# Kernel tuning notes

Hardware: AMD Instinct MI355X
Metric: run time of the kernel (lower is better)

## Reference

```python
import jax, jax.numpy as jnp
import numpy as np
from jax import lax

MU = 0.9      # params['momentum']
S = 0.1       # params['stepsize']
BETA = 0.999  # params['rnn_beta']
EPS = 1e-16   # self.eps

B, SEQ, IN, H = 64, 512, 512, 1024
G = 4 * H  # gates_size


def setup_inputs() -> dict:
    key = jax.random.key(0)
    ks = jax.random.split(key, 5)
    return {
        "x": jax.random.normal(ks[0], (B, SEQ, IN), dtype=jnp.float32),
        "weight_ih": jax.random.normal(ks[1], (IN, G), dtype=jnp.float32) * 0.05,
        "weight_hh": jax.random.normal(ks[2], (H, G), dtype=jnp.float32) * 0.05,
        "bias_ih": jax.random.normal(ks[3], (G,), dtype=jnp.float32) * 0.05,
        "bias_hh": jax.random.normal(ks[4], (G,), dtype=jnp.float32) * 0.05,
        "h0": jnp.zeros((B, H), dtype=jnp.float32),
        "c0": jnp.zeros((B, H), dtype=jnp.float32),
        "v0": jnp.zeros((B, G), dtype=jnp.float32),
        "m0": jnp.zeros((B, G), dtype=jnp.float32),
    }


def reference(x, weight_ih, weight_hh, bias_ih, bias_hh, h0, c0, v0, m0):
    # Precompute the input-to-gates projection for all timesteps in one GEMM.
    # grad_t = x_t @ W_ih + b_ih  -> [S, B, 4H] for scan
    grad_all = jnp.swapaxes(jnp.einsum('bsi,ig->bsg', x, weight_ih) + bias_ih, 0, 1)

    def step(carry, grad):
        h, c, v, m = carry
        v = MU * v + S * grad                       # momentum buffer
        m = BETA * m + (1.0 - BETA) * (grad * grad)  # second-moment buffer
        gates = v / (jnp.sqrt(m) + EPS) + h @ weight_hh + bias_hh
        i_g, f_g, g_g, o_g = jnp.split(gates, 4, axis=1)
        i_g = jax.nn.sigmoid(i_g)
        f_g = jax.nn.sigmoid(f_g)
        g_g = jnp.tanh(g_g)
        o_g = jax.nn.sigmoid(o_g)
        c = c * f_g + i_g * g_g
        h = o_g * jnp.tanh(c)
        return (h, c, v, m), h

    (h, c, v, m), ys = lax.scan(step, (h0, c0, v0, m0), grad_all)
    layer_output = jnp.swapaxes(ys, 0, 1)  # [B, S, H]
    return layer_output, h, c, v, m
```

## Files before the change

kernel.cpp:

```cpp
#include <hip/hip_runtime.h>
#include <cstdint>
#include <cstddef>

#define BB   64
#define SEQL 512
#define INF  512
#define HID  1024
#define GG   4096

#define MU_    0.9f
#define SSTEP_ 0.1f
#define BETA_  0.999f
#define EPS_   1e-16f
#define SCL    2048.0f
#define ISCL   (1.0f / 2048.0f)

#define NWGC  64
#define NWGP  128
#define NWG_TOT (NWGC + NWGP)
#define NTHR  1024
#define WLDS  131072
#define RLDS  32768
#define SMEM_BYTES (WLDS + RLDS)

typedef unsigned short u16;
typedef unsigned int   u32;
typedef unsigned long long u64;
typedef _Float16 half8 __attribute__((ext_vector_type(8)));
typedef float f32x4 __attribute__((ext_vector_type(4)));
typedef u32 u32x4 __attribute__((ext_vector_type(4)));

__device__ __forceinline__ f32x4 mfma16(half8 a, half8 b, f32x4 c) {
  return __builtin_amdgcn_mfma_f32_16x16x32_f16(a, b, c, 0, 0, 0);
}
__device__ __forceinline__ void fsplit(float v, _Float16& hi, _Float16& lo) {
  hi = (_Float16)v;
  lo = (_Float16)((v - (float)hi) * SCL);
}
__device__ __forceinline__ u32 coh_load32(const u32* p) {
  return __hip_atomic_load(p, __ATOMIC_RELAXED, __HIP_MEMORY_SCOPE_AGENT);
}
__device__ __forceinline__ void coh_store32(u32* p, u32 v) {
  __hip_atomic_store(p, v, __ATOMIC_RELAXED, __HIP_MEMORY_SCOPE_AGENT);
}
__device__ __forceinline__ void coh_store64(u64* p, u64 v) {
  __hip_atomic_store(p, v, __ATOMIC_RELAXED, __HIP_MEMORY_SCOPE_AGENT);
}
__device__ __forceinline__ void coh_storef(float* p, float v) {
  __hip_atomic_store(p, v, __ATOMIC_RELAXED, __HIP_MEMORY_SCOPE_AGENT);
}

#define GLD8(o0,o1,o2,o3,o4,o5,o6,o7,addr)                      \
  asm volatile(                                                 \
    "global_load_dwordx4 %0, %8, off sc0 sc1\n\t"               \
    "global_load_dwordx4 %1, %8, off offset:64 sc0 sc1\n\t"     \
    "global_load_dwordx4 %2, %8, off offset:128 sc0 sc1\n\t"    \
    "global_load_dwordx4 %3, %8, off offset:192 sc0 sc1\n\t"    \
    "global_load_dwordx4 %4, %8, off offset:256 sc0 sc1\n\t"    \
    "global_load_dwordx4 %5, %8, off offset:320 sc0 sc1\n\t"    \
    "global_load_dwordx4 %6, %8, off offset:384 sc0 sc1\n\t"    \
    "global_load_dwordx4 %7, %8, off offset:448 sc0 sc1"        \
    : "=&v"(o0), "=&v"(o1), "=&v"(o2), "=&v"(o3),               \
      "=&v"(o4), "=&v"(o5), "=&v"(o6), "=&v"(o7)                \
    : "v"(addr))

#define GLDU4(d0,d1,d2,d3,a0,a1,a2,a3)                          \
  asm volatile(                                                 \
    "global_load_dword %0, %4, off sc0 sc1\n\t"                 \
    "global_load_dword %1, %5, off sc0 sc1\n\t"                 \
    "global_load_dword %2, %6, off sc0 sc1\n\t"                 \
    "global_load_dword %3, %7, off sc0 sc1"                     \
    : "=&v"(d0), "=&v"(d1), "=&v"(d2), "=&v"(d3)                \
    : "v"(a0), "v"(a1), "v"(a2), "v"(a3))

#define HIMF(Hk, kk)                                                        \
  {                                                                         \
    half8 ah = __builtin_bit_cast(half8, Hk);                               \
    const _Float16* wb = Wf + (size_t)((kq * 8 + (kk)) * 4) * 512 + lane * 8;\
    a0 = mfma16(ah, *(const half8*)(wb), a0);                               \
    a1 = mfma16(ah, *(const half8*)(wb + 512), a1);                         \
    a2 = mfma16(ah, *(const half8*)(wb + 1024), a2);                        \
    a3 = mfma16(ah, *(const half8*)(wb + 1536), a3);                        \
  }

__global__ __launch_bounds__(256) void transpose_split(const float* __restrict__ src,
                                                       _Float16* __restrict__ dhi,
                                                       _Float16* __restrict__ dlo,
                                                       int R, int C) {
  __shared__ float tile[32][33];
  int c0 = blockIdx.x * 32, r0 = blockIdx.y * 32;
  int tx = threadIdx.x & 31, ty = threadIdx.x >> 5;
#pragma unroll
  for (int i = 0; i < 32; i += 8)
    tile[ty + i][tx] = src[(size_t)(r0 + ty + i) * C + (c0 + tx)];
  __syncthreads();
#pragma unroll
  for (int i = 0; i < 32; i += 8) {
    float v = tile[tx][ty + i];
    _Float16 hi, lo;
    fsplit(v, hi, lo);
    size_t o = (size_t)(c0 + ty + i) * R + (r0 + tx);
    dhi[o] = hi;
    dlo[o] = lo;
  }
}

__global__ __launch_bounds__(256) void split_x(const float* __restrict__ x,
                                               _Float16* __restrict__ xs) {
  size_t i = (size_t)blockIdx.x * 256 + threadIdx.x;
  size_t e = i * 8;
  size_t r = e / INF, col = e % INF;
  f32x4 v0 = *(const f32x4*)(x + e);
  f32x4 v1 = *(const f32x4*)(x + e + 4);
  half8 hi, lo;
#pragma unroll
  for (int j = 0; j < 4; j++) {
    _Float16 h_, l_;
    fsplit(v0[j], h_, l_); hi[j] = h_; lo[j] = l_;
    fsplit(v1[j], h_, l_); hi[4 + j] = h_; lo[4 + j] = l_;
  }
  _Float16* dst = xs + r * 2 * INF + col;
  *(half8*)(dst) = hi;
  *(half8*)(dst + INF) = lo;
}

__global__ __launch_bounds__(256) void init_state(const float* __restrict__ h0,
                                                  const float* __restrict__ c0,
                                                  const float* __restrict__ v0,
                                                  const float* __restrict__ m0,
                                                  float* __restrict__ co,
                                                  float* __restrict__ vo,
                                                  float* __restrict__ mo,
                                                  _Float16* __restrict__ hhi) {
  int i = blockIdx.x * 256 + threadIdx.x;
  if (i < BB * GG) { vo[i] = v0[i]; mo[i] = m0[i]; }
  if (i < BB * HID) {
    co[i] = c0[i];
    hhi[i] = (_Float16)h0[i];
  }
}

__global__ __attribute__((amdgpu_flat_work_group_size(NTHR, NTHR),
                          amdgpu_waves_per_eu(4, 4))) void rnn_fused(
    const _Float16* __restrict__ xs,
    const _Float16* __restrict__ whi,
    const _Float16* __restrict__ wlo,
    const float* __restrict__ bih,
    float* __restrict__ u,
    const _Float16* __restrict__ whh_hi,
    const float* __restrict__ bhh,
    _Float16* __restrict__ hA, _Float16* __restrict__ hB,
    float* __restrict__ lout, float* __restrict__ hout,
    float* __restrict__ cout,
    float* __restrict__ vst, float* __restrict__ mst,
    u32* __restrict__ flags, int t0, int T) {
  extern __shared__ char smem[];
  int tid = threadIdx.x;
  int wave = tid >> 6, lane = tid & 63;
  int l15 = lane & 15, lg = lane >> 4;

  if (blockIdx.x < NWGC) {
    _Float16* Wf = (_Float16*)smem;
    float* red = (float*)(smem + WLDS);
    u16* hpk = (u16*)(smem + WLDS);
    int bt = wave >> 2, kq = wave & 3;
    int nb = blockIdx.x;

    for (int s = tid; s < 8192; s += NTHR) {
      int ln = s & 63, rest = s >> 6;
      int rt = rest & 3, kk = (rest >> 2) & 7, kq2 = rest >> 5;
      int grow = rt * HID + nb * 16 + (ln & 15);
      int k = kq2 * 256 + kk * 32 + (ln >> 4) * 8;
      *(half8*)(Wf + (size_t)s * 8) = *(const half8*)(whh_hi + (size_t)grow * HID + k);
    }

    int bo = tid >> 4, j = tid & 15;
    int en = nb * 16 + j;
    int within = bo & 15, btE = bo >> 4;
    int wsl = (((within >> 2) + j) & 3) * 4 + (within & 3);
    float bh_[4], creg;
#pragma unroll
    for (int q = 0; q < 4; q++) bh_[q] = bhh[q * HID + en];
    creg = cout[(size_t)bo * HID + en];
    u64 hOffB = (u64)(((bt * 16 + l15) * HID + kq * 256 + lg * 8) * 2);
    u64 hAB = (u64)(uintptr_t)hA + hOffB;
    u64 hBB = (u64)(uintptr_t)hB + hOffB;
    int sb = tid >> 2, ss = tid & 3;
    u64* stA = (u64*)(hA + (size_t)sb * HID + nb * 16) + ss;
    u64* stB = (u64*)(hB + (size_t)sb * HID + nb * 16) + ss;
    u64 ubT = (u64)(uintptr_t)u + (((size_t)bo * GG) + en) * 4;
    __syncthreads();

    if (wave == 0) {
      u32 tp = (u32)(t0 + (T < 2 ? T : 2));
      const u32* p0 = flags + (size_t)(NWGC + 2 * lane) * 32;
      while (!__all(coh_load32(p0) >= tp && coh_load32(p0 + 32) >= tp))
        __builtin_amdgcn_s_sleep(1);
    }
    __syncthreads();
    float uv0, uv1, uv2, uv3;
    GLDU4(uv0, uv1, uv2, uv3, ubT, ubT + 4096, ubT + 8192, ubT + 12288);
    asm volatile("s_waitcnt vmcnt(0)"
                 : "+v"(uv0), "+v"(uv1), "+v"(uv2), "+v"(uv3) :: "memory");
    float uv[4] = {uv0, uv1, uv2, uv3};

    for (int tt = 0; tt < T; ++tt) {
      int gt = t0 + tt;
      u64 rB = (gt & 1) ? hBB : hAB;

      u32x4 H0, H1, H2, H3, H4, H5, H6, H7;
      GLD8(H0, H1, H2, H3, H4, H5, H6, H7, rB);
      asm volatile("s_waitcnt vmcnt(0)" ::: "memory");
      __builtin_amdgcn_sched_barrier(0);

      f32x4 a0 = {}, a1 = {}, a2 = {}, a3 = {};
      HIMF(H0, 0) HIMF(H1, 1) HIMF(H2, 2) HIMF(H3, 3)
      HIMF(H4, 4) HIMF(H5, 5) HIMF(H6, 6) HIMF(H7, 7)

      int kqh = kq >> 1;
      int p = (lg + l15) & 3;
      int sB0 = (((bt * 2 + kqh) * 4 + 0) * 16 + l15) * 16 + p * 4;
      int sB1 = (((bt * 2 + kqh) * 4 + 1) * 16 + l15) * 16 + p * 4;
      int sB2 = (((bt * 2 + kqh) * 4 + 2) * 16 + l15) * 16 + p * 4;
      int sB3 = (((bt * 2 + kqh) * 4 + 3) * 16 + l15) * 16 + p * 4;
      if (kq & 1) {
        *(f32x4*)(red + sB0) = a0;
        *(f32x4*)(red + sB1) = a1;
        *(f32x4*)(red + sB2) = a2;
        *(f32x4*)(red + sB3) = a3;
      }
      __syncthreads();
      if (!(kq & 1)) {
        *(f32x4*)(red + sB0) = a0 + *(const f32x4*)(red + sB0);
        *(f32x4*)(red + sB1) = a1 + *(const f32x4*)(red + sB1);
        *(f32x4*)(red + sB2) = a2 + *(const f32x4*)(red + sB2);
        *(f32x4*)(red + sB3) = a3 + *(const f32x4*)(red + sB3);
      }
      float uvN0 = 0, uvN1 = 0, uvN2 = 0, uvN3 = 0;
      if (tt + 1 < T) {
        u64 ubn = ubT + ((u64)(tt + 1) * ((u64)BB * GG * 4));
        GLDU4(uvN0, uvN1, uvN2, uvN3, ubn, ubn + 4096, ubn + 8192, ubn + 12288);
      }
      __syncthreads();

      float gate[4];
#pragma unroll
      for (int q = 0; q < 4; q++) {
        float rec = red[(((btE * 2 + 0) * 4 + q) * 16 + j) * 16 + wsl] +
                    red[(((btE * 2 + 1) * 4 + q) * 16 + j) * 16 + wsl];
        gate[q] = uv[q] + rec + bh_[q];
      }
      float ig = 1.0f / (1.0f + expf(-gate[0]));
      float fg = 1.0f / (1.0f + expf(-gate[1]));
      float gg = tanhf(gate[2]);
      float og = 1.0f / (1.0f + expf(-gate[3]));
      creg = creg * fg + ig * gg;
      float hh = og * tanhf(creg);
      __syncthreads();

      lout[((size_t)bo * SEQL + gt) * HID + en] = hh;
      hpk[bo * 16 + j] = __builtin_bit_cast(u16, (_Float16)hh);
      if (gt == SEQL - 1) hout[(size_t)bo * HID + en] = hh;
      if (tt == T - 1)    cout[(size_t)bo * HID + en] = creg;
      __syncthreads();

      if (tid < 256) {
        u64 val = *(const u64*)(hpk + sb * 16 + ss * 4);
        coh_store64((gt & 1) ? stA : stB, val);
      }

      if (tt + 1 < T) {
        asm volatile("s_waitcnt vmcnt(0)"
                     : "+v"(uvN0), "+v"(uvN1), "+v"(uvN2), "+v"(uvN3) :: "memory");
        __syncthreads();
        u32 target = (u32)(t0 + tt + 1);
        if (tid == 0) coh_store32(flags + (size_t)nb * 32, target);
        if (wave == 0) {
          const u32* f0 = flags + (size_t)lane * 32;
          while (!__all(coh_load32(f0) >= target))
            __builtin_amdgcn_s_sleep(1);
        } else if (wave == 1) {
          u32 t2 = (u32)(t0 + (tt + 3 < T ? tt + 3 : T));
          const u32* p0 = flags + (size_t)(NWGC + 2 * lane) * 32;
          while (!__all(coh_load32(p0) >= t2 && coh_load32(p0 + 32) >= t2))
            __builtin_amdgcn_s_sleep(1);
        }
        __syncthreads();
        uv[0] = uvN0; uv[1] = uvN1; uv[2] = uvN2; uv[3] = uvN3;
      }
    }
  } else {
    float* pred = (float*)smem;
    int pid = blockIdx.x - NWGC;
    int btp = pid & 3;
    int n0 = (pid >> 2) * 128;
    int nt = wave & 7, kh = wave >> 3;

    const _Float16* xa = xs + (size_t)(btp * 16 + l15) * SEQL * (2 * INF)
                            + kh * 256 + lg * 8;
    const _Float16* whp = whi + (size_t)(n0 + nt * 16 + l15) * INF + kh * 256 + lg * 8;
    const _Float16* wlp = wlo + (size_t)(n0 + nt * 16 + l15) * INF + kh * 256 + lg * 8;
    float* pp = pred + (((kh * 8 + nt) * 16 + l15) * 16 + lg * 4);

    int b_l = tid >> 6, g_l = tid & 63;
    int bg = btp * 16 + b_l;
    int g0 = n0 + g_l, g1 = n0 + g_l + 64;
    size_t gi0 = (size_t)bg * GG + g0, gi1 = (size_t)bg * GG + g1;
    float vr0 = vst[gi0], vr1 = vst[gi1];
    float mr0 = mst[gi0], mr1 = mst[gi1];
    float bi0 = bih[g0], bi1 = bih[g1];
    int nt0 = g_l >> 4, c0i = g_l & 15;
    int nt1 = (g_l + 64) >> 4, c1i = g_l & 15;
    __syncthreads();

    for (int tt = 0; tt < T; ++tt) {
      const _Float16* xt = xa + (size_t)(t0 + tt) * (2 * INF);
      f32x4 aM = {}, aL = {};
#pragma unroll
      for (int kk = 0; kk < 256; kk += 32) {
        half8 ah = *(const half8*)(xt + kk);
        half8 al = *(const half8*)(xt + INF + kk);
        half8 bh = *(const half8*)(whp + kk);
        half8 bl = *(const half8*)(wlp + kk);
        aM = mfma16(ah, bh, aM);
        aL = mfma16(al, bh, aL);
        aL = mfma16(ah, bl, aL);
      }
      f32x4 cb;
#pragma unroll
      for (int i2 = 0; i2 < 4; ++i2) cb[i2] = aM[i2] + aL[i2] * ISCL;
      *(f32x4*)pp = cb;
      __syncthreads();

      float rec0 = pred[((0 + nt0) * 16 + c0i) * 16 + b_l] +
                   pred[((8 + nt0) * 16 + c0i) * 16 + b_l];
      float rec1 = pred[((0 + nt1) * 16 + c1i) * 16 + b_l] +
                   pred[((8 + nt1) * 16 + c1i) * 16 + b_l];
      float gr0 = rec0 + bi0, gr1 = rec1 + bi1;
      vr0 = MU_ * vr0 + SSTEP_ * gr0;
      mr0 = BETA_ * mr0 + (1.0f - BETA_) * gr0 * gr0;
      vr1 = MU_ * vr1 + SSTEP_ * gr1;
      mr1 = BETA_ * mr1 + (1.0f - BETA_) * gr1 * gr1;
      float* ub = u + ((size_t)tt * BB + bg) * GG;
      coh_storef(ub + g0, vr0 / (sqrtf(mr0) + EPS_));
      coh_storef(ub + g1, vr1 / (sqrtf(mr1) + EPS_));
      if (tt == T - 1) {
        vst[gi0] = vr0; vst[gi1] = vr1;
        mst[gi0] = mr0; mst[gi1] = mr1;
      }
      asm volatile("s_waitcnt vmcnt(0)" ::: "memory");
      __syncthreads();
      if (tid == 0)
        coh_store32(flags + (size_t)(NWGC + pid) * 32, (u32)(t0 + tt + 1));
    }
  }
}

extern "C" void kernel_launch(void* const* d_in, const int* in_sizes, int n_in,
                              void* d_out, int out_size, void* d_ws, size_t ws_size,
                              hipStream_t stream) {
  const float* x   = (const float*)d_in[0];
  const float* wih = (const float*)d_in[1];
  const float* whh = (const float*)d_in[2];
  const float* bih = (const float*)d_in[3];
  const float* bhh = (const float*)d_in[4];
  const float* h0  = (const float*)d_in[5];
  const float* c0  = (const float*)d_in[6];
  const float* v0  = (const float*)d_in[7];
  const float* m0  = (const float*)d_in[8];

  float* out  = (float*)d_out;
  float* lout = out;
  float* hout = out + (size_t)BB * SEQL * HID;
  float* cout = hout + (size_t)BB * HID;
  float* vout = cout + (size_t)BB * HID;
  float* mout = vout + (size_t)BB * GG;

  char* ws = (char*)d_ws;
  size_t o = 0;
  _Float16* wih_hi = (_Float16*)(ws + o); o += (size_t)GG * INF * 2;
  _Float16* wih_lo = (_Float16*)(ws + o); o += (size_t)GG * INF * 2;
  _Float16* whh_hi = (_Float16*)(ws + o); o += (size_t)GG * HID * 2;
  _Float16* whh_lo = (_Float16*)(ws + o); o += (size_t)GG * HID * 2;
  _Float16* xs     = (_Float16*)(ws + o); o += (size_t)BB * SEQL * 2 * INF * 2;
  _Float16* hA     = (_Float16*)(ws + o); o += (size_t)BB * HID * 2;
  _Float16* hB     = (_Float16*)(ws + o); o += (size_t)BB * HID * 2;
  o = (o + 255) & ~(size_t)255;
  u32* flags = (u32*)(ws + o); o += (size_t)NWG_TOT * 32 * 4;
  float* U = (float*)(ws + o);

  const size_t STEP_BYTES = (size_t)BB * GG * sizeof(float);
  size_t cap = (ws_size > o) ? (ws_size - o) / STEP_BYTES : 1;
  if (cap < 1) cap = 1;
  int Tc = (int)(cap < (size_t)SEQL ? cap : (size_t)SEQL);

  split_x<<<(BB * SEQL * INF / 8) / 256, 256, 0, stream>>>(x, xs);
  transpose_split<<<dim3(GG / 32, INF / 32), 256, 0, stream>>>(wih, wih_hi, wih_lo, INF, GG);
  transpose_split<<<dim3(GG / 32, HID / 32), 256, 0, stream>>>(whh, whh_hi, whh_lo, HID, GG);
  init_state<<<(BB * GG) / 256, 256, 0, stream>>>(h0, c0, v0, m0, cout, vout, mout, hA);
  hipMemsetAsync(flags, 0, (size_t)NWG_TOT * 32 * 4, stream);

  for (int t0 = 0; t0 < SEQL; t0 += Tc) {
    int T = (SEQL - t0 < Tc) ? (SEQL - t0) : Tc;
    rnn_fused<<<NWG_TOT, NTHR, SMEM_BYTES, stream>>>(
        xs, wih_hi, wih_lo, bih, U, whh_hi, bhh,
        hA, hB, lout, hout, cout, vout, mout, flags, t0, T);
  }
}
```

Baseline: 4.585 ms.

## Replace per-step flag barrier with timestep-tagged hidden-state words polled directly

Each fp16 hidden value is stored in a 32-bit word with the timestep tag in the upper half. Consumer workgroups spin on the hidden-state loads until every tag matches the current step, which removes the separate flag store, all-workgroup flag poll and extra syncthreads per timestep. The next-step U prefetch is issued earlier and the producer-progress wait is moved after the MFMAs. This doubles the bytes read and written for h each step and adds unpack work. Correctness depends on the per-word tagging holding across buffer reuse.

Measured after the change: 6.119 ms. 33.5% more time.

```diff
diff --git a/kernel.cpp b/kernel.cpp
--- a/kernel.cpp
+++ b/kernel.cpp
@@ -50,19 +50,29 @@
   __hip_atomic_store(p, v, __ATOMIC_RELAXED, __HIP_MEMORY_SCOPE_AGENT);
 }
 
-#define GLD8(o0,o1,o2,o3,o4,o5,o6,o7,addr)                      \
-  asm volatile(                                                 \
-    "global_load_dwordx4 %0, %8, off sc0 sc1\n\t"               \
-    "global_load_dwordx4 %1, %8, off offset:64 sc0 sc1\n\t"     \
-    "global_load_dwordx4 %2, %8, off offset:128 sc0 sc1\n\t"    \
-    "global_load_dwordx4 %3, %8, off offset:192 sc0 sc1\n\t"    \
-    "global_load_dwordx4 %4, %8, off offset:256 sc0 sc1\n\t"    \
-    "global_load_dwordx4 %5, %8, off offset:320 sc0 sc1\n\t"    \
-    "global_load_dwordx4 %6, %8, off offset:384 sc0 sc1\n\t"    \
-    "global_load_dwordx4 %7, %8, off offset:448 sc0 sc1"        \
-    : "=&v"(o0), "=&v"(o1), "=&v"(o2), "=&v"(o3),               \
-      "=&v"(o4), "=&v"(o5), "=&v"(o6), "=&v"(o7)                \
-    : "v"(addr))
+#define GLD16(P0,P1,P2,P3,P4,P5,P6,P7,P8,P9,Pa,Pb,Pc,Pd,Pe,Pf,PA)  \
+  asm volatile(                                                     \
+    "global_load_dwordx4 %0, %16, off sc0 sc1\n\t"                  \
+    "global_load_dwordx4 %1, %16, off offset:16 sc0 sc1\n\t"        \
+    "global_load_dwordx4 %2, %16, off offset:128 sc0 sc1\n\t"       \
+    "global_load_dwordx4 %3, %16, off offset:144 sc0 sc1\n\t"       \
+    "global_load_dwordx4 %4, %16, off offset:256 sc0 sc1\n\t"       \
+    "global_load_dwordx4 %5, %16, off offset:272 sc0 sc1\n\t"       \
+    "global_load_dwordx4 %6, %16, off offset:384 sc0 sc1\n\t"       \
+    "global_load_dwordx4 %7, %16, off offset:400 sc0 sc1\n\t"       \
+    "global_load_dwordx4 %8, %16, off offset:512 sc0 sc1\n\t"       \
+    "global_load_dwordx4 %9, %16, off offset:528 sc0 sc1\n\t"       \
+    "global_load_dwordx4 %10, %16, off offset:640 sc0 sc1\n\t"      \
+    "global_load_dwordx4 %11, %16, off offset:656 sc0 sc1\n\t"      \
+    "global_load_dwordx4 %12, %16, off offset:768 sc0 sc1\n\t"      \
+    "global_load_dwordx4 %13, %16, off offset:784 sc0 sc1\n\t"      \
+    "global_load_dwordx4 %14, %16, off offset:896 sc0 sc1\n\t"      \
+    "global_load_dwordx4 %15, %16, off offset:912 sc0 sc1"          \
+    : "=&v"(P0), "=&v"(P1), "=&v"(P2), "=&v"(P3),                   \
+      "=&v"(P4), "=&v"(P5), "=&v"(P6), "=&v"(P7),                   \
+      "=&v"(P8), "=&v"(P9), "=&v"(Pa), "=&v"(Pb),                   \
+      "=&v"(Pc), "=&v"(Pd), "=&v"(Pe), "=&v"(Pf)                    \
+    : "v"(PA))
 
 #define GLDU4(d0,d1,d2,d3,a0,a1,a2,a3)                          \
   asm volatile(                                                 \
@@ -73,14 +83,18 @@
     : "=&v"(d0), "=&v"(d1), "=&v"(d2), "=&v"(d3)                \
     : "v"(a0), "v"(a1), "v"(a2), "v"(a3))
 
-#define HIMF(Hk, kk)                                                        \
+#define UNPK_MFMA(W0, W1, kk)                                               \
   {                                                                         \
-    half8 ah = __builtin_bit_cast(half8, Hk);                               \
+    union { u16 e[8]; half8 h8; } A_;                                       \
+    A_.e[0] = (u16)(W0)[0]; A_.e[1] = (u16)(W0)[1];                         \
+    A_.e[2] = (u16)(W0)[2]; A_.e[3] = (u16)(W0)[3];                         \
+    A_.e[4] = (u16)(W1)[0]; A_.e[5] = (u16)(W1)[1];                         \
+    A_.e[6] = (u16)(W1)[2]; A_.e[7] = (u16)(W1)[3];                         \
     const _Float16* wb = Wf + (size_t)((kq * 8 + (kk)) * 4) * 512 + lane * 8;\
-    a0 = mfma16(ah, *(const half8*)(wb), a0);                               \
-    a1 = mfma16(ah, *(const half8*)(wb + 512), a1);                         \
-    a2 = mfma16(ah, *(const half8*)(wb + 1024), a2);                        \
-    a3 = mfma16(ah, *(const half8*)(wb + 1536), a3);                        \
+    a0 = mfma16(A_.h8, *(const half8*)(wb), a0);                            \
+    a1 = mfma16(A_.h8, *(const half8*)(wb + 512), a1);                      \
+    a2 = mfma16(A_.h8, *(const half8*)(wb + 1024), a2);                     \
+    a3 = mfma16(A_.h8, *(const half8*)(wb + 1536), a3);                     \
   }
 
 __global__ __launch_bounds__(256) void transpose_split(const float* __restrict__ src,
@@ -131,12 +145,15 @@
                                                   float* __restrict__ co,
                                                   float* __restrict__ vo,
                                                   float* __restrict__ mo,
-                                                  _Float16* __restrict__ hhi) {
+                                                  u32* __restrict__ hT0,
+                                                  u32* __restrict__ hT1) {
   int i = blockIdx.x * 256 + threadIdx.x;
   if (i < BB * GG) { vo[i] = v0[i]; mo[i] = m0[i]; }
   if (i < BB * HID) {
     co[i] = c0[i];
-    hhi[i] = (_Float16)h0[i];
+    u16 hb = __builtin_bit_cast(u16, (_Float16)h0[i]);
+    hT0[i] = (u32)hb;
+    hT1[i] = 0xFFFF0000u;
   }
 }
 
@@ -149,7 +166,7 @@
     float* __restrict__ u,
     const _Float16* __restrict__ whh_hi,
     const float* __restrict__ bhh,
-    _Float16* __restrict__ hA, _Float16* __restrict__ hB,
+    u32* __restrict__ hTA, u32* __restrict__ hTB,
     float* __restrict__ lout, float* __restrict__ hout,
     float* __restrict__ cout,
     float* __restrict__ vst, float* __restrict__ mst,
@@ -162,7 +179,7 @@
   if (blockIdx.x < NWGC) {
     _Float16* Wf = (_Float16*)smem;
     float* red = (float*)(smem + WLDS);
-    u16* hpk = (u16*)(smem + WLDS);
+    u32* hpk = (u32*)(smem + WLDS);
     int bt = wave >> 2, kq = wave & 3;
     int nb = blockIdx.x;
 
@@ -182,12 +199,12 @@
 #pragma unroll
     for (int q = 0; q < 4; q++) bh_[q] = bhh[q * HID + en];
     creg = cout[(size_t)bo * HID + en];
-    u64 hOffB = (u64)(((bt * 16 + l15) * HID + kq * 256 + lg * 8) * 2);
-    u64 hAB = (u64)(uintptr_t)hA + hOffB;
-    u64 hBB = (u64)(uintptr_t)hB + hOffB;
-    int sb = tid >> 2, ss = tid & 3;
-    u64* stA = (u64*)(hA + (size_t)sb * HID + nb * 16) + ss;
-    u64* stB = (u64*)(hB + (size_t)sb * HID + nb * 16) + ss;
+    u64 hOffB = (u64)(((bt * 16 + l15) * HID + kq * 256 + lg * 8) * 4);
+    u64 hTA_ = (u64)(uintptr_t)hTA + hOffB;
+    u64 hTB_ = (u64)(uintptr_t)hTB + hOffB;
+    int sb = tid >> 3, ss = tid & 7;
+    u64* wA = (u64*)(hTA + (size_t)sb * HID + nb * 16) + ss;
+    u64* wB = (u64*)(hTB + (size_t)sb * HID + nb * 16) + ss;
     u64 ubT = (u64)(uintptr_t)u + (((size_t)bo * GG) + en) * 4;
     __syncthreads();
 
@@ -198,24 +215,49 @@
         __builtin_amdgcn_s_sleep(1);
     }
     __syncthreads();
-    float uv0, uv1, uv2, uv3;
-    GLDU4(uv0, uv1, uv2, uv3, ubT, ubT + 4096, ubT + 8192, ubT + 12288);
+    float uvA, uvB, uvC, uvD;
+    GLDU4(uvA, uvB, uvC, uvD, ubT, ubT + 4096, ubT + 8192, ubT + 12288);
     asm volatile("s_waitcnt vmcnt(0)"
-                 : "+v"(uv0), "+v"(uv1), "+v"(uv2), "+v"(uv3) :: "memory");
-    float uv[4] = {uv0, uv1, uv2, uv3};
+                 : "+v"(uvA), "+v"(uvB), "+v"(uvC), "+v"(uvD) :: "memory");
+    float uv[4] = {uvA, uvB, uvC, uvD};
 
     for (int tt = 0; tt < T; ++tt) {
       int gt = t0 + tt;
-      u64 rB = (gt & 1) ? hBB : hAB;
-
-      u32x4 H0, H1, H2, H3, H4, H5, H6, H7;
-      GLD8(H0, H1, H2, H3, H4, H5, H6, H7, rB);
-      asm volatile("s_waitcnt vmcnt(0)" ::: "memory");
-      __builtin_amdgcn_sched_barrier(0);
+      u64 rB = (gt & 1) ? hTB_ : hTA_;
+      u32 key = ((u32)gt & 0xFFFFu) << 16;
+      u32x4 key4 = {key, key, key, key};
+
+      u32x4 T0, T1, T2, T3, T4, T5, T6, T7, T8, T9, Ta, Tb, Tc_, Td, Te, Tf;
+      while (true) {
+        GLD16(T0, T1, T2, T3, T4, T5, T6, T7, T8, T9, Ta, Tb, Tc_, Td, Te, Tf, rB);
+        asm volatile("s_waitcnt vmcnt(0)" ::: "memory");
+        __builtin_amdgcn_sched_barrier(0);
+        u32x4 b4 = (T0 ^ key4) | (T1 ^ key4) | (T2 ^ key4) | (T3 ^ key4) |
+                   (T4 ^ key4) | (T5 ^ key4) | (T6 ^ key4) | (T7 ^ key4) |
+                   (T8 ^ key4) | (T9 ^ key4) | (Ta ^ key4) | (Tb ^ key4) |
+                   (Tc_ ^ key4) | (Td ^ key4) | (Te ^ key4) | (Tf ^ key4);
+        u32 bad = (b4[0] | b4[1] | b4[2] | b4[3]) >> 16;
+        if (__all(bad == 0)) break;
+        __builtin_amdgcn_s_sleep(1);
+      }
+      float uvN0 = 0, uvN1 = 0, uvN2 = 0, uvN3 = 0;
+      if (tt + 1 < T) {
+        u64 ubn = ubT + ((u64)(tt + 1) * ((u64)BB * GG * 4));
+        GLDU4(uvN0, uvN1, uvN2, uvN3, ubn, ubn + 4096, ubn + 8192, ubn + 12288);
+      }
 
       f32x4 a0 = {}, a1 = {}, a2 = {}, a3 = {};
-      HIMF(H0, 0) HIMF(H1, 1) HIMF(H2, 2) HIMF(H3, 3)
-      HIMF(H4, 4) HIMF(H5, 5) HIMF(H6, 6) HIMF(H7, 7)
+      UNPK_MFMA(T0, T1, 0) UNPK_MFMA(T2, T3, 1)
+      UNPK_MFMA(T4, T5, 2) UNPK_MFMA(T6, T7, 3)
+      UNPK_MFMA(T8, T9, 4) UNPK_MFMA(Ta, Tb, 5)
+      UNPK_MFMA(Tc_, Td, 6) UNPK_MFMA(Te, Tf, 7)
+
+      if (wave == 1) {
+        u32 t2 = (u32)(t0 + (tt + 3 < T ? tt + 3 : T));
+        const u32* p0 = flags + (size_t)(NWGC + 2 * lane) * 32;
+        while (!__all(coh_load32(p0) >= t2 && coh_load32(p0 + 32) >= t2))
+          __builtin_amdgcn_s_sleep(1);
+      }
 
       int kqh = kq >> 1;
       int p = (lg + l15) & 3;
@@ -236,11 +278,6 @@
         *(f32x4*)(red + sB2) = a2 + *(const f32x4*)(red + sB2);
         *(f32x4*)(red + sB3) = a3 + *(const f32x4*)(red + sB3);
       }
-      float uvN0 = 0, uvN1 = 0, uvN2 = 0, uvN3 = 0;
-      if (tt + 1 < T) {
-        u64 ubn = ubT + ((u64)(tt + 1) * ((u64)BB * GG * 4));
-        GLDU4(uvN0, uvN1, uvN2, uvN3, ubn, ubn + 4096, ubn + 8192, ubn + 12288);
-      }
       __syncthreads();
 
       float gate[4];
@@ -250,6 +287,10 @@
                     red[(((btE * 2 + 1) * 4 + q) * 16 + j) * 16 + wsl];
         gate[q] = uv[q] + rec + bh_[q];
       }
+      asm volatile("s_waitcnt vmcnt(0)"
+                   : "+v"(uvN0), "+v"(uvN1), "+v"(uvN2), "+v"(uvN3) :: "memory");
+      uv[0] = uvN0; uv[1] = uvN1; uv[2] = uvN2; uv[3] = uvN3;
+
       float ig = 1.0f / (1.0f + expf(-gate[0]));
       float fg = 1.0f / (1.0f + expf(-gate[1]));
       float gg = tanhf(gate[2]);
@@ -259,34 +300,15 @@
       __syncthreads();
 
       lout[((size_t)bo * SEQL + gt) * HID + en] = hh;
-      hpk[bo * 16 + j] = __builtin_bit_cast(u16, (_Float16)hh);
+      hpk[bo * 16 + j] = (u32)__builtin_bit_cast(u16, (_Float16)hh) |
+                         ((u32)((gt + 1) & 0xFFFF) << 16);
       if (gt == SEQL - 1) hout[(size_t)bo * HID + en] = hh;
       if (tt == T - 1)    cout[(size_t)bo * HID + en] = creg;
       __syncthreads();
 
-      if (tid < 256) {
-        u64 val = *(const u64*)(hpk + sb * 16 + ss * 4);
-        coh_store64((gt & 1) ? stA : stB, val);
-      }
-
-      if (tt + 1 < T) {
-        asm volatile("s_waitcnt vmcnt(0)"
-                     : "+v"(uvN0), "+v"(uvN1), "+v"(uvN2), "+v"(uvN3) :: "memory");
-        __syncthreads();
-        u32 target = (u32)(t0 + tt + 1);
-        if (tid == 0) coh_store32(flags + (size_t)nb * 32, target);
-        if (wave == 0) {
-          const u32* f0 = flags + (size_t)lane * 32;
-          while (!__all(coh_load32(f0) >= target))
-            __builtin_amdgcn_s_sleep(1);
-        } else if (wave == 1) {
-          u32 t2 = (u32)(t0 + (tt + 3 < T ? tt + 3 : T));
-          const u32* p0 = flags + (size_t)(NWGC + 2 * lane) * 32;
-          while (!__all(coh_load32(p0) >= t2 && coh_load32(p0 + 32) >= t2))
-            __builtin_amdgcn_s_sleep(1);
-        }
-        __syncthreads();
-        uv[0] = uvN0; uv[1] = uvN1; uv[2] = uvN2; uv[3] = uvN3;
+      if (tid < 512) {
+        u64 val = *(const u64*)(hpk + sb * 16 + ss * 2);
+        coh_store64((gt & 1) ? wA : wB, val);
       }
     }
   } else {
@@ -383,8 +405,8 @@
   _Float16* whh_hi = (_Float16*)(ws + o); o += (size_t)GG * HID * 2;
   _Float16* whh_lo = (_Float16*)(ws + o); o += (size_t)GG * HID * 2;
   _Float16* xs     = (_Float16*)(ws + o); o += (size_t)BB * SEQL * 2 * INF * 2;
-  _Float16* hA     = (_Float16*)(ws + o); o += (size_t)BB * HID * 2;
-  _Float16* hB     = (_Float16*)(ws + o); o += (size_t)BB * HID * 2;
+  u32* hTA = (u32*)(ws + o); o += (size_t)BB * HID * 4;
+  u32* hTB = (u32*)(ws + o); o += (size_t)BB * HID * 4;
   o = (o + 255) & ~(size_t)255;
   u32* flags = (u32*)(ws + o); o += (size_t)NWG_TOT * 32 * 4;
   float* U = (float*)(ws + o);
@@ -397,13 +419,13 @@
   split_x<<<(BB * SEQL * INF / 8) / 256, 256, 0, stream>>>(x, xs);
   transpose_split<<<dim3(GG / 32, INF / 32), 256, 0, stream>>>(wih, wih_hi, wih_lo, INF, GG);
   transpose_split<<<dim3(GG / 32, HID / 32), 256, 0, stream>>>(whh, whh_hi, whh_lo, HID, GG);
-  init_state<<<(BB * GG) / 256, 256, 0, stream>>>(h0, c0, v0, m0, cout, vout, mout, hA);
+  init_state<<<(BB * GG) / 256, 256, 0, stream>>>(h0, c0, v0, m0, cout, vout, mout, hTA, hTB);
   hipMemsetAsync(flags, 0, (size_t)NWG_TOT * 32 * 4, stream);
 
   for (int t0 = 0; t0 < SEQL; t0 += Tc) {
     int T = (SEQL - t0 < Tc) ? (SEQL - t0) : Tc;
     rnn_fused<<<NWG_TOT, NTHR, SMEM_BYTES, stream>>>(
         xs, wih_hi, wih_lo, bih, U, whh_hi, bhh,
-        hA, hB, lout, hout, cout, vout, mout, flags, t0, T);
-  }
-}
+        hTA, hTB, lout, hout, cout, vout, mout, flags, t0, T);
+  }
+}
```
